# Performance work log

Hardware: AMD Instinct MI355X
Metric: run time of the kernel (lower is better)

The kernel has to match this reference:

```python
import jax, jax.numpy as jnp
import numpy as np

EMBED = 768
HEAD = 64
SEQ = 4096
BATCH = 4


def setup_inputs() -> dict:
    key = jax.random.key(0)
    ks = jax.random.split(key, 7)
    s = 1.0 / np.sqrt(EMBED)
    x = jax.random.normal(ks[0], (BATCH, SEQ, EMBED), dtype=jnp.float32)
    Wq = jax.random.uniform(ks[1], (EMBED, HEAD), jnp.float32, -s, s)
    bq = jax.random.uniform(ks[2], (HEAD,), jnp.float32, -s, s)
    Wk = jax.random.uniform(ks[3], (EMBED, HEAD), jnp.float32, -s, s)
    bk = jax.random.uniform(ks[4], (HEAD,), jnp.float32, -s, s)
    Wv = jax.random.uniform(ks[5], (EMBED, HEAD), jnp.float32, -s, s)
    bv = jax.random.uniform(ks[6], (HEAD,), jnp.float32, -s, s)
    return {"x": x, "Wq": Wq, "bq": bq, "Wk": Wk, "bk": bk, "Wv": Wv, "bv": bv}


def reference(x, Wq, bq, Wk, bk, Wv, bv):
    # x: [B,T,E]
    Q = x @ Wq + bq  # [B,T,H]
    K = x @ Wk + bk
    V = x @ Wv + bv
    scale = 1.0 / jnp.sqrt(jnp.asarray(HEAD, dtype=x.dtype))
    wei = jnp.einsum('bqh,bkh->bqk', Q, K) * scale  # [B,T,T]
    T = x.shape[1]
    causal = jnp.tril(jnp.ones((T, T), dtype=bool))
    wei = jnp.where(causal, wei, -jnp.inf)
    wei = jax.nn.softmax(wei, axis=-1)
    return jnp.einsum('bqk,bkh->bqh', wei, V)  # [B,T,H]
```

## Files before the change

### kernel.cpp

```cpp
#include <hip/hip_runtime.h>


#define BB 4
#define TT 4096
#define EE 768
#define HH 64
#define BT (BB*TT)

typedef __attribute__((ext_vector_type(8))) short short8;
typedef __attribute__((ext_vector_type(4))) float f32x4;
#define MFMA16(a,b,c) __builtin_amdgcn_mfma_f32_16x16x32_bf16(a,b,c,0,0,0)
#define QSCALE 0.18033688011112042f

static __device__ __forceinline__ float bflo(unsigned a){ return __uint_as_float(a << 16); }
static __device__ __forceinline__ unsigned short f2bf(float f){
    unsigned x = __float_as_uint(f);
    x += 0x7fffu + ((x >> 16) & 1u);
    return (unsigned short)(x >> 16);
}
template<int FP32>
static __device__ __forceinline__ float ldin(const void* p, int idx){
    if (FP32) return ((const float*)p)[idx];
    return bflo(((const unsigned short*)p)[idx]);
}

template<int FP32>
static __device__ void wt_body(const void* W, int wi, int e0, unsigned short* wt){
    __shared__ unsigned short ts[64 * 72];
    const int tid = threadIdx.x;
    #pragma unroll
    for (int p = 0; p < 2; p++){
        int i = p * 256 + tid;
        int r = i >> 3, g = i & 7;
        unsigned short v[8];
        if (FP32){
            const float* src = (const float*)W + (size_t)(e0 + r) * HH + g * 8;
            const float4 a = *(const float4*)src, b = *(const float4*)(src + 4);
            v[0]=f2bf(a.x); v[1]=f2bf(a.y); v[2]=f2bf(a.z); v[3]=f2bf(a.w);
            v[4]=f2bf(b.x); v[5]=f2bf(b.y); v[6]=f2bf(b.z); v[7]=f2bf(b.w);
        } else {
            const unsigned short* src = (const unsigned short*)W + (size_t)(e0 + r) * HH + g * 8;
            #pragma unroll
            for (int j = 0; j < 8; j++) v[j] = src[j];
        }
        #pragma unroll
        for (int j = 0; j < 8; j++) ts[r * 72 + g * 8 + j] = v[j];
    }
    __syncthreads();
    #pragma unroll
    for (int p = 0; p < 2; p++){
        int i = p * 256 + tid;
        int h = i >> 3, g = i & 7;
        unsigned short v[8];
        #pragma unroll
        for (int j = 0; j < 8; j++) v[j] = ts[(g * 8 + j) * 72 + h];
        unsigned short* dst = wt + (size_t)(wi * 64 + h) * EE + e0 + g * 8;
        uint4 pk;
        pk.x = (unsigned)v[0] | ((unsigned)v[1] << 16);
        pk.y = (unsigned)v[2] | ((unsigned)v[3] << 16);
        pk.z = (unsigned)v[4] | ((unsigned)v[5] << 16);
        pk.w = (unsigned)v[6] | ((unsigned)v[7] << 16);
        *(uint4*)dst = pk;
    }
}
__global__ __launch_bounds__(256) void wt_kernel(
    const unsigned short* xu, const void* Wq, const void* Wk, const void* Wv,
    unsigned short* wt, int* flag){
    __shared__ int cnt;
    const int tid = threadIdx.x;
    if (tid == 0) cnt = 0;
    __syncthreads();
    int c = 0;
    #pragma unroll
    for (int i = 0; i < 16; i++){
        unsigned u = xu[tid * 16 + i];
        unsigned e = (u >> 7) & 0xFFu;
        if (e >= 140u) c++;
    }
    atomicAdd(&cnt, c);
    __syncthreads();
    const int fp32 = (cnt > 32) ? 1 : 0;
    if (blockIdx.x == 0 && tid == 0) *flag = fp32;
    const int wi = blockIdx.x / 12;
    const int e0 = (blockIdx.x % 12) * 64;
    const void* W = (wi == 0) ? Wq : (wi == 1) ? Wk : Wv;
    if (fp32) wt_body<1>(W, wi, e0, wt);
    else      wt_body<0>(W, wi, e0, wt);
}

template<int FP32>
static __device__ void qkv_body(const void* x, const unsigned short* wt,
    const void* bq, const void* bk, const void* bv,
    unsigned short* Qw, unsigned short* Kw, unsigned short* VTw,
    unsigned short* xs, unsigned short* wsl)
{
    const int tid = threadIdx.x, lane = tid & 63, w = tid >> 6;
    const int l15 = lane & 15, quad = lane >> 4;
    const int z = blockIdx.x;
    const int m0 = (z >> 1) * 32;
    const int nh = z & 1;
    const int rh = (w & 1) * 16;
    const int ngl = (w >> 1) * 3;

    f32x4 acc[3];
    #pragma unroll
    for (int i = 0; i < 3; i++) acc[i] = (f32x4)(0.f);

    const int srow = tid >> 3, sg = tid & 7;

    for (int c = 0; c < 12; c++){
        const int c0 = c * 64;
        __syncthreads();
        {
            short8 v;
            if (FP32){
                const float* src = (const float*)x + (size_t)(m0 + srow) * EE + c0 + sg * 8;
                const float4 a = *(const float4*)src, b2 = *(const float4*)(src + 4);
                v[0]=(short)f2bf(a.x); v[1]=(short)f2bf(a.y); v[2]=(short)f2bf(a.z); v[3]=(short)f2bf(a.w);
                v[4]=(short)f2bf(b2.x); v[5]=(short)f2bf(b2.y); v[6]=(short)f2bf(b2.z); v[7]=(short)f2bf(b2.w);
            } else {
                v = *(const short8*)((const unsigned short*)x + (size_t)(m0 + srow) * EE + c0 + sg * 8);
            }
            *(short8*)&xs[srow * 72 + sg * 8] = v;
        }
        #pragma unroll
        for (int p = 0; p < 3; p++){
            int i = p * 256 + tid;
            int n = i >> 3, g2 = i & 7;
            *(short8*)&wsl[n * 72 + g2 * 8] =
                *(const short8*)(wt + (size_t)(nh * 96 + n) * EE + c0 + g2 * 8);
        }
        __syncthreads();
        #pragma unroll
        for (int kst = 0; kst < 2; kst++){
            const short8 a = *(const short8*)&xs[(rh + l15) * 72 + kst * 32 + quad * 8];
            #pragma unroll
            for (int nf = 0; nf < 3; nf++){
                const short8 bfr = *(const short8*)&wsl[((ngl + nf) * 16 + l15) * 72 + kst * 32 + quad * 8];
                acc[nf] = MFMA16(a, bfr, acc[nf]);
            }
        }
    }
    #pragma unroll
    for (int nf = 0; nf < 3; nf++){
        const int gi = nh * 6 + ngl + nf;
        const int wi = gi >> 2;
        const int h = (gi & 3) * 16 + l15;
        const void* bp = (wi == 0) ? bq : (wi == 1) ? bk : bv;
        const float bias = ldin<FP32>(bp, h);
        if (wi == 0){
            #pragma unroll
            for (int rr = 0; rr < 4; rr++){
                const int tok = m0 + rh + quad * 4 + rr;
                Qw[(size_t)tok * HH + h] = f2bf((acc[nf][rr] + bias) * QSCALE);
            }
        } else if (wi == 1){
            #pragma unroll
            for (int rr = 0; rr < 4; rr++){
                const int tok = m0 + rh + quad * 4 + rr;
                Kw[(size_t)tok * HH + h] = f2bf(acc[nf][rr] + bias);
            }
        } else {
            const int tok0 = m0 + rh + quad * 4;
            const int bloc = tok0 >> 12;
            const int tl = tok0 & 4095;
            uint2 pk;
            pk.x = (unsigned)f2bf(acc[nf][0] + bias) | ((unsigned)f2bf(acc[nf][1] + bias) << 16);
            pk.y = (unsigned)f2bf(acc[nf][2] + bias) | ((unsigned)f2bf(acc[nf][3] + bias) << 16);
            *(uint2*)&VTw[(size_t)(bloc * 64 + h) * TT + tl] = pk;
        }
    }
}
__global__ __launch_bounds__(256, 4) void qkv_kernel(
    const void* x, const unsigned short* wt,
    const void* bq, const void* bk, const void* bv,
    unsigned short* Qw, unsigned short* Kw, unsigned short* VTw, const int* flag){
    __shared__ unsigned short xs[32 * 72];
    __shared__ unsigned short wsl[96 * 72];
    if (*flag) qkv_body<1>(x, wt, bq, bk, bv, Qw, Kw, VTw, xs, wsl);
    else       qkv_body<0>(x, wt, bq, bk, bv, Qw, Kw, VTw, xs, wsl);
}

__global__ __launch_bounds__(512, 2) void attn_kernel(
    const unsigned short* __restrict__ Q,
    const unsigned short* __restrict__ K, const unsigned short* __restrict__ VT,
    void* __restrict__ out, const int* __restrict__ flag)
{
    __shared__ unsigned short sbuf[8][2304];
    __shared__ float lpart[8][32];

    const int mode = *flag;
    const int z = blockIdx.x;
    const int b = z & 3;
    const int qt = 127 - (z >> 2);
    const int q0 = qt * 32;
    const int nkb = (qt >> 1) + 1;
    const int tid = threadIdx.x;
    const int lane = tid & 63;
    const int w = tid >> 6;
    const int l15 = lane & 15, quad = lane >> 4;
    const int brow = b * TT;

    f32x4 O[2][4];
    float lsum[2][4];
    #pragma unroll
    for (int mt = 0; mt < 2; mt++)
        #pragma unroll
        for (int i = 0; i < 4; i++){ O[mt][i] = (f32x4)(0.f); lsum[mt][i] = 0.f; }

    if (w < nkb){
        short8 qf[2][2];
        #pragma unroll
        for (int mt = 0; mt < 2; mt++)
            #pragma unroll
            for (int kst = 0; kst < 2; kst++)
                qf[mt][kst] = *(const short8*)(Q + (size_t)(brow + q0 + mt * 16 + l15) * HH + kst * 32 + quad * 8);

        short8 kf[4][2];
        #pragma unroll
        for (int c = 0; c < 4; c++)
            #pragma unroll
            for (int kst = 0; kst < 2; kst++)
                kf[c][kst] = *(const short8*)(K + (size_t)(brow + w * 64 + c * 16 + l15) * HH + kst * 32 + quad * 8);

        for (int u = w; u < nkb; u += 8){
            const int k0 = u * 64;
            f32x4 sacc[2][4];
            #pragma unroll
            for (int mt = 0; mt < 2; mt++)
                #pragma unroll
                for (int c = 0; c < 4; c++){
                    sacc[mt][c] = (f32x4)(0.f);
                    sacc[mt][c] = MFMA16(qf[mt][0], kf[c][0], sacc[mt][c]);
                    sacc[mt][c] = MFMA16(qf[mt][1], kf[c][1], sacc[mt][c]);
                }
            short8 vf[4][2];
            #pragma unroll
            for (int c = 0; c < 4; c++)
                #pragma unroll
                for (int kst = 0; kst < 2; kst++)
                    vf[c][kst] = *(const short8*)(VT + (size_t)(b * 64 + c * 16 + l15) * TT + k0 + kst * 32 + quad * 8);
            if (u + 8 < nkb){
                const int kn0 = (u + 8) * 64;
                #pragma unroll
                for (int c = 0; c < 4; c++)
                    #pragma unroll
                    for (int kst = 0; kst < 2; kst++)
                        kf[c][kst] = *(const short8*)(K + (size_t)(brow + kn0 + c * 16 + l15) * HH + kst * 32 + quad * 8);
            }
            const bool diag = (u == nkb - 1);
            #pragma unroll
            for (int mt = 0; mt < 2; mt++){
                #pragma unroll
                for (int c = 0; c < 4; c++){
                    #pragma unroll
                    for (int rr = 0; rr < 4; rr++){
                        float sv = sacc[mt][c][rr];
                        if (diag){
                            const int kg = k0 + c * 16 + l15;
                            const int qg = q0 + mt * 16 + quad * 4 + rr;
                            sv = (kg <= qg) ? sv : -1e30f;
                        }
                        const float p = exp2f(sv);
                        lsum[mt][rr] += p;
                        sbuf[w][mt * 1152 + (quad * 4 + rr) * 72 + c * 16 + l15] = f2bf(p);
                    }
                }
            }
            #pragma unroll
            for (int mt = 0; mt < 2; mt++){
                const short8 pf0 = *(const short8*)&sbuf[w][mt * 1152 + l15 * 72 + quad * 8];
                const short8 pf1 = *(const short8*)&sbuf[w][mt * 1152 + l15 * 72 + 32 + quad * 8];
                #pragma unroll
                for (int c2 = 0; c2 < 4; c2++){
                    O[mt][c2] = MFMA16(pf0, vf[c2][0], O[mt][c2]);
                    O[mt][c2] = MFMA16(pf1, vf[c2][1], O[mt][c2]);
                }
            }
        }
        #pragma unroll
        for (int mt = 0; mt < 2; mt++)
            #pragma unroll
            for (int rr = 0; rr < 4; rr++){
                #pragma unroll
                for (int off = 1; off < 16; off <<= 1)
                    lsum[mt][rr] += __shfl_xor(lsum[mt][rr], off, 64);
            }
    }
    #pragma unroll
    for (int mt = 0; mt < 2; mt++)
        #pragma unroll
        for (int rr = 0; rr < 4; rr++){
            const int row = mt * 16 + quad * 4 + rr;
            #pragma unroll
            for (int c2 = 0; c2 < 4; c2++)
                sbuf[w][row * 72 + c2 * 16 + l15] = f2bf(O[mt][c2][rr]);
            if (l15 == 0) lpart[w][row] = lsum[mt][rr];
        }
    __syncthreads();
    #pragma unroll
    for (int i = 0; i < 4; i++){
        const int e = i * 512 + tid;
        const int r = e >> 6, h = e & 63;
        float num = 0.f, den = 0.f;
        #pragma unroll
        for (int ww = 0; ww < 8; ww++){
            num += bflo(sbuf[ww][r * 72 + h]);
            den += lpart[ww][r];
        }
        const float ov = num / den;
        const size_t gi = (size_t)(brow + q0 + r) * HH + h;
        if (mode) ((float*)out)[gi] = ov;
        else      ((unsigned short*)out)[gi] = f2bf(ov);
    }
}

extern "C" void kernel_launch(void* const* d_in, const int* in_sizes, int n_in,
                              void* d_out, int out_size, void* d_ws, size_t ws_size,
                              hipStream_t stream) {
    const void* x  = d_in[0];
    const void* Wq = d_in[1];
    const void* bq = d_in[2];
    const void* Wk = d_in[3];
    const void* bk = d_in[4];
    const void* Wv = d_in[5];
    const void* bv = d_in[6];

    unsigned short* Qw  = (unsigned short*)d_ws;
    unsigned short* Kw  = Qw + (size_t)BT * HH;
    unsigned short* VTw = Kw + (size_t)BT * HH;
    unsigned short* wt  = VTw + (size_t)BT * HH;
    int* flag  = (int*)(wt + (size_t)192 * EE);

    wt_kernel<<<36, 256, 0, stream>>>((const unsigned short*)x, Wq, Wk, Wv, wt, flag);
    qkv_kernel<<<1024, 256, 0, stream>>>(x, wt, bq, bk, bv, Qw, Kw, VTw, flag);
    attn_kernel<<<512, 512, 0, stream>>>(Qw, Kw, VTw, d_out, flag);
}
```

Before: 159.4 us.

## Pair high and low query tiles per attention block; widen QKV projection tiles

The attention kernel now handles two query tiles per block, a long one (127-pz) and a short one (pz). This balances causal work across blocks and reuses each loaded K and V tile for both query tiles. The QKV projection block now computes all 192 output columns for its 32 rows, so each x tile is loaded and converted once instead of twice. The costs are higher register pressure from two sets of accumulators, a larger LDS weight buffer, and half as many blocks in each kernel, which may lower occupancy or tail parallelism.

```diff
diff --git a/kernel.cpp b/kernel.cpp
--- a/kernel.cpp
+++ b/kernel.cpp
@@ -96,15 +96,13 @@
 {
     const int tid = threadIdx.x, lane = tid & 63, w = tid >> 6;
     const int l15 = lane & 15, quad = lane >> 4;
-    const int z = blockIdx.x;
-    const int m0 = (z >> 1) * 32;
-    const int nh = z & 1;
+    const int m0 = blockIdx.x * 32;
     const int rh = (w & 1) * 16;
-    const int ngl = (w >> 1) * 3;
-
-    f32x4 acc[3];
-    #pragma unroll
-    for (int i = 0; i < 3; i++) acc[i] = (f32x4)(0.f);
+    const int ngl = (w >> 1) * 6;
+
+    f32x4 acc[6];
+    #pragma unroll
+    for (int i = 0; i < 6; i++) acc[i] = (f32x4)(0.f);
 
     const int srow = tid >> 3, sg = tid & 7;
 
@@ -124,26 +122,26 @@
             *(short8*)&xs[srow * 72 + sg * 8] = v;
         }
         #pragma unroll
-        for (int p = 0; p < 3; p++){
+        for (int p = 0; p < 6; p++){
             int i = p * 256 + tid;
             int n = i >> 3, g2 = i & 7;
             *(short8*)&wsl[n * 72 + g2 * 8] =
-                *(const short8*)(wt + (size_t)(nh * 96 + n) * EE + c0 + g2 * 8);
+                *(const short8*)(wt + (size_t)n * EE + c0 + g2 * 8);
         }
         __syncthreads();
         #pragma unroll
         for (int kst = 0; kst < 2; kst++){
             const short8 a = *(const short8*)&xs[(rh + l15) * 72 + kst * 32 + quad * 8];
             #pragma unroll
-            for (int nf = 0; nf < 3; nf++){
+            for (int nf = 0; nf < 6; nf++){
                 const short8 bfr = *(const short8*)&wsl[((ngl + nf) * 16 + l15) * 72 + kst * 32 + quad * 8];
                 acc[nf] = MFMA16(a, bfr, acc[nf]);
             }
         }
     }
     #pragma unroll
-    for (int nf = 0; nf < 3; nf++){
-        const int gi = nh * 6 + ngl + nf;
+    for (int nf = 0; nf < 6; nf++){
+        const int gi = ngl + nf;
         const int wi = gi >> 2;
         const int h = (gi & 3) * 16 + l15;
         const void* bp = (wi == 0) ? bq : (wi == 1) ? bk : bv;
@@ -176,9 +174,58 @@
     const void* bq, const void* bk, const void* bv,
     unsigned short* Qw, unsigned short* Kw, unsigned short* VTw, const int* flag){
     __shared__ unsigned short xs[32 * 72];
-    __shared__ unsigned short wsl[96 * 72];
+    __shared__ unsigned short wsl[192 * 72];
     if (*flag) qkv_body<1>(x, wt, bq, bk, bv, Qw, Kw, VTw, xs, wsl);
     else       qkv_body<0>(x, wt, bq, bk, bv, Qw, Kw, VTw, xs, wsl);
+}
+
+static __device__ __forceinline__ void qk_mfma(
+    const short8 (&qf)[2][2], const short8 (&kf)[4][2], f32x4 (&s)[2][4])
+{
+    #pragma unroll
+    for (int mt = 0; mt < 2; mt++)
+        #pragma unroll
+        for (int c = 0; c < 4; c++){
+            s[mt][c] = (f32x4)(0.f);
+            s[mt][c] = MFMA16(qf[mt][0], kf[c][0], s[mt][c]);
+            s[mt][c] = MFMA16(qf[mt][1], kf[c][1], s[mt][c]);
+        }
+}
+static __device__ __forceinline__ void softmax_store(
+    f32x4 (&sacc)[2][4], unsigned short* sb, float (&lsum)[2][4],
+    bool diag, int k0, int q0, int l15, int quad)
+{
+    #pragma unroll
+    for (int mt = 0; mt < 2; mt++)
+        #pragma unroll
+        for (int c = 0; c < 4; c++)
+            #pragma unroll
+            for (int rr = 0; rr < 4; rr++){
+                float sv = sacc[mt][c][rr];
+                if (diag){
+                    const int kg = k0 + c * 16 + l15;
+                    const int qg = q0 + mt * 16 + quad * 4 + rr;
+                    sv = (kg <= qg) ? sv : -1e30f;
+                }
+                const float p = exp2f(sv);
+                lsum[mt][rr] += p;
+                sb[mt * 1152 + (quad * 4 + rr) * 72 + c * 16 + l15] = f2bf(p);
+            }
+}
+static __device__ __forceinline__ void pv_accum(
+    const unsigned short* sb, const short8 (&vf)[4][2], f32x4 (&O)[2][4],
+    int l15, int quad)
+{
+    #pragma unroll
+    for (int mt = 0; mt < 2; mt++){
+        const short8 pf0 = *(const short8*)&sb[mt * 1152 + l15 * 72 + quad * 8];
+        const short8 pf1 = *(const short8*)&sb[mt * 1152 + l15 * 72 + 32 + quad * 8];
+        #pragma unroll
+        for (int c2 = 0; c2 < 4; c2++){
+            O[mt][c2] = MFMA16(pf0, vf[c2][0], O[mt][c2]);
+            O[mt][c2] = MFMA16(pf1, vf[c2][1], O[mt][c2]);
+        }
+    }
 }
 
 __global__ __launch_bounds__(512, 2) void attn_kernel(
@@ -192,101 +239,82 @@
     const int mode = *flag;
     const int z = blockIdx.x;
     const int b = z & 3;
-    const int qt = 127 - (z >> 2);
-    const int q0 = qt * 32;
-    const int nkb = (qt >> 1) + 1;
+    const int pz = z >> 2;
+    const int qtH = 127 - pz;
+    const int qtL = pz;
+    const int q0H = qtH * 32, q0L = qtL * 32;
+    const int nkbH = (qtH >> 1) + 1;
+    const int nkbL = (qtL >> 1) + 1;
     const int tid = threadIdx.x;
     const int lane = tid & 63;
     const int w = tid >> 6;
     const int l15 = lane & 15, quad = lane >> 4;
     const int brow = b * TT;
 
-    f32x4 O[2][4];
-    float lsum[2][4];
-    #pragma unroll
-    for (int mt = 0; mt < 2; mt++)
-        #pragma unroll
-        for (int i = 0; i < 4; i++){ O[mt][i] = (f32x4)(0.f); lsum[mt][i] = 0.f; }
-
-    if (w < nkb){
-        short8 qf[2][2];
-        #pragma unroll
-        for (int mt = 0; mt < 2; mt++)
+    f32x4 OH[2][4], OL[2][4];
+    float lsH[2][4], lsL[2][4];
+    #pragma unroll
+    for (int mt = 0; mt < 2; mt++)
+        #pragma unroll
+        for (int i = 0; i < 4; i++){
+            OH[mt][i] = (f32x4)(0.f); OL[mt][i] = (f32x4)(0.f);
+            lsH[mt][i] = 0.f; lsL[mt][i] = 0.f;
+        }
+
+    short8 qfH[2][2], qfL[2][2];
+    #pragma unroll
+    for (int mt = 0; mt < 2; mt++)
+        #pragma unroll
+        for (int kst = 0; kst < 2; kst++){
+            qfH[mt][kst] = *(const short8*)(Q + (size_t)(brow + q0H + mt * 16 + l15) * HH + kst * 32 + quad * 8);
+            qfL[mt][kst] = *(const short8*)(Q + (size_t)(brow + q0L + mt * 16 + l15) * HH + kst * 32 + quad * 8);
+        }
+
+    short8 kf[4][2];
+    #pragma unroll
+    for (int c = 0; c < 4; c++)
+        #pragma unroll
+        for (int kst = 0; kst < 2; kst++)
+            kf[c][kst] = *(const short8*)(K + (size_t)(brow + w * 64 + c * 16 + l15) * HH + kst * 32 + quad * 8);
+
+    for (int u = w; u < nkbH; u += 8){
+        const int k0 = u * 64;
+        const bool doL = (u < nkbL);
+        f32x4 sacc[2][4];
+        qk_mfma(qfH, kf, sacc);
+        short8 vf[4][2];
+        #pragma unroll
+        for (int c = 0; c < 4; c++)
             #pragma unroll
             for (int kst = 0; kst < 2; kst++)
-                qf[mt][kst] = *(const short8*)(Q + (size_t)(brow + q0 + mt * 16 + l15) * HH + kst * 32 + quad * 8);
-
-        short8 kf[4][2];
-        #pragma unroll
-        for (int c = 0; c < 4; c++)
-            #pragma unroll
-            for (int kst = 0; kst < 2; kst++)
-                kf[c][kst] = *(const short8*)(K + (size_t)(brow + w * 64 + c * 16 + l15) * HH + kst * 32 + quad * 8);
-
-        for (int u = w; u < nkb; u += 8){
-            const int k0 = u * 64;
-            f32x4 sacc[2][4];
-            #pragma unroll
-            for (int mt = 0; mt < 2; mt++)
-                #pragma unroll
-                for (int c = 0; c < 4; c++){
-                    sacc[mt][c] = (f32x4)(0.f);
-                    sacc[mt][c] = MFMA16(qf[mt][0], kf[c][0], sacc[mt][c]);
-                    sacc[mt][c] = MFMA16(qf[mt][1], kf[c][1], sacc[mt][c]);
-                }
-            short8 vf[4][2];
+                vf[c][kst] = *(const short8*)(VT + (size_t)(b * 64 + c * 16 + l15) * TT + k0 + kst * 32 + quad * 8);
+        softmax_store(sacc, &sbuf[w][0], lsH, (u == nkbH - 1), k0, q0H, l15, quad);
+        f32x4 saccL[2][4];
+        if (doL) qk_mfma(qfL, kf, saccL);
+        if (u + 8 < nkbH){
+            const int kn0 = (u + 8) * 64;
             #pragma unroll
             for (int c = 0; c < 4; c++)
                 #pragma unroll
                 for (int kst = 0; kst < 2; kst++)
-                    vf[c][kst] = *(const short8*)(VT + (size_t)(b * 64 + c * 16 + l15) * TT + k0 + kst * 32 + quad * 8);
-            if (u + 8 < nkb){
-                const int kn0 = (u + 8) * 64;
-                #pragma unroll
-                for (int c = 0; c < 4; c++)
-                    #pragma unroll
-                    for (int kst = 0; kst < 2; kst++)
-                        kf[c][kst] = *(const short8*)(K + (size_t)(brow + kn0 + c * 16 + l15) * HH + kst * 32 + quad * 8);
-            }
-            const bool diag = (u == nkb - 1);
-            #pragma unroll
-            for (int mt = 0; mt < 2; mt++){
-                #pragma unroll
-                for (int c = 0; c < 4; c++){
-                    #pragma unroll
-                    for (int rr = 0; rr < 4; rr++){
-                        float sv = sacc[mt][c][rr];
-                        if (diag){
-                            const int kg = k0 + c * 16 + l15;
-                            const int qg = q0 + mt * 16 + quad * 4 + rr;
-                            sv = (kg <= qg) ? sv : -1e30f;
-                        }
-                        const float p = exp2f(sv);
-                        lsum[mt][rr] += p;
-                        sbuf[w][mt * 1152 + (quad * 4 + rr) * 72 + c * 16 + l15] = f2bf(p);
-                    }
-                }
-            }
-            #pragma unroll
-            for (int mt = 0; mt < 2; mt++){
-                const short8 pf0 = *(const short8*)&sbuf[w][mt * 1152 + l15 * 72 + quad * 8];
-                const short8 pf1 = *(const short8*)&sbuf[w][mt * 1152 + l15 * 72 + 32 + quad * 8];
-                #pragma unroll
-                for (int c2 = 0; c2 < 4; c2++){
-                    O[mt][c2] = MFMA16(pf0, vf[c2][0], O[mt][c2]);
-                    O[mt][c2] = MFMA16(pf1, vf[c2][1], O[mt][c2]);
-                }
-            }
-        }
-        #pragma unroll
-        for (int mt = 0; mt < 2; mt++)
-            #pragma unroll
-            for (int rr = 0; rr < 4; rr++){
-                #pragma unroll
-                for (int off = 1; off < 16; off <<= 1)
-                    lsum[mt][rr] += __shfl_xor(lsum[mt][rr], off, 64);
-            }
-    }
+                    kf[c][kst] = *(const short8*)(K + (size_t)(brow + kn0 + c * 16 + l15) * HH + kst * 32 + quad * 8);
+        }
+        pv_accum(&sbuf[w][0], vf, OH, l15, quad);
+        if (doL){
+            softmax_store(saccL, &sbuf[w][0], lsL, (u == nkbL - 1), k0, q0L, l15, quad);
+            pv_accum(&sbuf[w][0], vf, OL, l15, quad);
+        }
+    }
+    #pragma unroll
+    for (int mt = 0; mt < 2; mt++)
+        #pragma unroll
+        for (int rr = 0; rr < 4; rr++){
+            #pragma unroll
+            for (int off = 1; off < 16; off <<= 1){
+                lsH[mt][rr] += __shfl_xor(lsH[mt][rr], off, 64);
+                lsL[mt][rr] += __shfl_xor(lsL[mt][rr], off, 64);
+            }
+        }
     #pragma unroll
     for (int mt = 0; mt < 2; mt++)
         #pragma unroll
@@ -294,8 +322,8 @@
             const int row = mt * 16 + quad * 4 + rr;
             #pragma unroll
             for (int c2 = 0; c2 < 4; c2++)
-                sbuf[w][row * 72 + c2 * 16 + l15] = f2bf(O[mt][c2][rr]);
-            if (l15 == 0) lpart[w][row] = lsum[mt][rr];
+                sbuf[w][row * 72 + c2 * 16 + l15] = f2bf(OH[mt][c2][rr]);
+            if (l15 == 0) lpart[w][row] = lsH[mt][rr];
         }
     __syncthreads();
     #pragma unroll
@@ -309,7 +337,34 @@
             den += lpart[ww][r];
         }
         const float ov = num / den;
-        const size_t gi = (size_t)(brow + q0 + r) * HH + h;
+        const size_t gi = (size_t)(brow + q0H + r) * HH + h;
+        if (mode) ((float*)out)[gi] = ov;
+        else      ((unsigned short*)out)[gi] = f2bf(ov);
+    }
+    __syncthreads();
+    #pragma unroll
+    for (int mt = 0; mt < 2; mt++)
+        #pragma unroll
+        for (int rr = 0; rr < 4; rr++){
+            const int row = mt * 16 + quad * 4 + rr;
+            #pragma unroll
+            for (int c2 = 0; c2 < 4; c2++)
+                sbuf[w][row * 72 + c2 * 16 + l15] = f2bf(OL[mt][c2][rr]);
+            if (l15 == 0) lpart[w][row] = lsL[mt][rr];
+        }
+    __syncthreads();
+    #pragma unroll
+    for (int i = 0; i < 4; i++){
+        const int e = i * 512 + tid;
+        const int r = e >> 6, h = e & 63;
+        float num = 0.f, den = 0.f;
+        #pragma unroll
+        for (int ww = 0; ww < 8; ww++){
+            num += bflo(sbuf[ww][r * 72 + h]);
+            den += lpart[ww][r];
+        }
+        const float ov = num / den;
+        const size_t gi = (size_t)(brow + q0L + r) * HH + h;
         if (mode) ((float*)out)[gi] = ov;
         else      ((unsigned short*)out)[gi] = f2bf(ov);
     }
@@ -333,6 +388,6 @@
     int* flag  = (int*)(wt + (size_t)192 * EE);
 
     wt_kernel<<<36, 256, 0, stream>>>((const unsigned short*)x, Wq, Wk, Wv, wt, flag);
-    qkv_kernel<<<1024, 256, 0, stream>>>(x, wt, bq, bk, bv, Qw, Kw, VTw, flag);
-    attn_kernel<<<512, 512, 0, stream>>>(Qw, Kw, VTw, d_out, flag);
-}
+    qkv_kernel<<<512, 256, 0, stream>>>(x, wt, bq, bk, bv, Qw, Kw, VTw, flag);
+    attn_kernel<<<256, 512, 0, stream>>>(Qw, Kw, VTw, d_out, flag);
+}
```

After: 169.8 us. 6.5% more time.
